# Performance work log

Hardware: AMD Instinct MI355X
Metric: run time of the kernel (lower is better)

The kernel has to match this reference:

```python
import jax, jax.numpy as jnp
import numpy as np

B, NQ, NK, DQ, DK, DV, H = 8, 256, 512, 256, 256, 256, 64
NEG = -1e6


def setup_inputs() -> dict:
    key = jax.random.key(0)
    k1, k2, k3, k4, k5, k6, k7 = jax.random.split(key, 7)
    return {
        "queries": jax.random.normal(k1, (B, NQ, DQ), dtype=jnp.float32),
        "keys": jax.random.normal(k2, (B, NK, DK), dtype=jnp.float32),
        "values": jax.random.normal(k3, (B, NK, DV), dtype=jnp.float32),
        "valid_lens": jax.random.randint(k4, (B,), 1, NK + 1),
        "Wq": jax.random.normal(k5, (DQ, H), dtype=jnp.float32) / np.sqrt(DQ),
        "Wk": jax.random.normal(k6, (DK, H), dtype=jnp.float32) / np.sqrt(DK),
        "wv": jax.random.normal(k7, (H,), dtype=jnp.float32) / np.sqrt(H),
    }


def reference(queries, keys, values, valid_lens, Wq, Wk, wv):
    # project: [B,NQ,H], [B,NK,H]
    q = jnp.einsum("bqd,dh->bqh", queries, Wq)
    k = jnp.einsum("bkd,dh->bkh", keys, Wk)
    # additive features: [B,NQ,NK,H] -> tanh -> reduce with w_v -> scores [B,NQ,NK]
    features = jnp.tanh(q[:, :, None, :] + k[:, None, :, :])
    scores = jnp.einsum("bqkh,h->bqk", features, wv)
    # masked softmax over key axis (per-batch valid_lens)
    mask = jnp.arange(NK)[None, None, :] < valid_lens[:, None, None]
    scores = jnp.where(mask, scores, NEG)
    attn = jax.nn.softmax(scores, axis=-1)
    # dropout p=0 (eval) -> identity; weighted sum of values [B,NQ,DV]
    return jnp.einsum("bqk,bkv->bqv", attn, values)
```

## Files before the change

### kernel.cpp

```cpp
#include <hip/hip_runtime.h>
#include <hip/hip_bf16.h>

constexpr int B  = 8;
constexpr int NQ = 256;
constexpr int NK = 512;
constexpr int D  = 256;
constexpr int DV = 256;
constexpr int H  = 64;
constexpr float NEG = -1e6f;
constexpr float LOG2E = 1.4426950408889634f;
constexpr float CSCALE = 2.f * LOG2E;

constexpr int RPB = 32;

__global__ __launch_bounds__(512) void proj_kernel(
    const float* __restrict__ queries, const float* __restrict__ keys,
    const float* __restrict__ Wq, const float* __restrict__ Wk,
    float* __restrict__ qp, float* __restrict__ kp)
{
    const int r0 = blockIdx.x * RPB;
    const bool isQ = (r0 < B * NQ);
    const float* src = isQ ? queries + (size_t)r0 * D
                           : keys + (size_t)(r0 - B * NQ) * D;
    const float* W   = isQ ? Wq : Wk;
    float* out       = isQ ? qp + (size_t)r0 * H
                           : kp + (size_t)(r0 - B * NQ) * H;

    __shared__ __align__(16) float rows[RPB][D];
#pragma unroll
    for (int j = 0; j < 4; ++j)
        ((float4*)&rows[0][0])[threadIdx.x + j * 512] =
            ((const float4*)src)[threadIdx.x + j * 512];
    __syncthreads();

    const int h = threadIdx.x & 63;
    const int g = threadIdx.x >> 6;
    float s0 = 0.f, s1 = 0.f, s2 = 0.f, s3 = 0.f;
#pragma unroll 2
    for (int d4 = 0; d4 < D / 4; ++d4) {
        float w0 = W[(d4 * 4 + 0) * H + h];
        float w1 = W[(d4 * 4 + 1) * H + h];
        float w2 = W[(d4 * 4 + 2) * H + h];
        float w3 = W[(d4 * 4 + 3) * H + h];
        float4 ra = *(const float4*)&rows[g][d4 * 4];
        float4 rb = *(const float4*)&rows[g + 8][d4 * 4];
        float4 rc = *(const float4*)&rows[g + 16][d4 * 4];
        float4 rd = *(const float4*)&rows[g + 24][d4 * 4];
        s0 = fmaf(ra.x, w0, s0);  s1 = fmaf(rb.x, w0, s1);
        s2 = fmaf(rc.x, w0, s2);  s3 = fmaf(rd.x, w0, s3);
        s0 = fmaf(ra.y, w1, s0);  s1 = fmaf(rb.y, w1, s1);
        s2 = fmaf(rc.y, w1, s2);  s3 = fmaf(rd.y, w1, s3);
        s0 = fmaf(ra.z, w2, s0);  s1 = fmaf(rb.z, w2, s1);
        s2 = fmaf(rc.z, w2, s2);  s3 = fmaf(rd.z, w2, s3);
        s0 = fmaf(ra.w, w3, s0);  s1 = fmaf(rb.w, w3, s1);
        s2 = fmaf(rc.w, w3, s2);  s3 = fmaf(rd.w, w3, s3);
    }
    out[g * H + h]         = s0 * CSCALE;
    out[(g + 8) * H + h]   = s1 * CSCALE;
    out[(g + 16) * H + h]  = s2 * CSCALE;
    out[(g + 24) * H + h]  = s3 * CSCALE;
}

constexpr int KT   = 128;
constexpr int KPAD = 68;

#define FMA4(acc, a, v) \
    acc.x = fmaf(a, v.x, acc.x); acc.y = fmaf(a, v.y, acc.y); \
    acc.z = fmaf(a, v.z, acc.z); acc.w = fmaf(a, v.w, acc.w);

__global__ __launch_bounds__(512, 4) void attn_kernel(
    const float* __restrict__ qp, const float* __restrict__ kp,
    const float* __restrict__ values, const int* __restrict__ valid_lens,
    const float* __restrict__ wv, float* __restrict__ out)
{
    const int b    = blockIdx.x & 7;
    const int q0   = (blockIdx.x >> 3) * 4;
    const int t    = threadIdx.x;
    const int w    = t >> 6;
    const int l    = t & 63;
    const int qloc = w >> 1;
    const int half = w & 1;

    __shared__ __align__(16) float kT[KT * KPAD];
    __shared__ __align__(16) float qv[4][H];
    __shared__ __align__(16) float w2[H];
    __shared__ __align__(16) float sc[4][NK];

    if (half == 0)
        qv[qloc][l] = qp[((size_t)b * NQ + q0 + qloc) * H + l];

    const float wvl = wv[l];
    float swv = wvl;
#pragma unroll
    for (int off = 32; off > 0; off >>= 1) swv += __shfl_xor(swv, off);
    if (w == 0) w2[l] = -2.f * wvl;

    const int vlen = valid_lens[b];

    for (int kt = 0; kt < NK / KT; ++kt) {
        const int kg = kt * KT + half * 64 + l;
        if (kt * KT < vlen) {
            __syncthreads();
            const float* src = kp + ((size_t)b * NK + kt * KT) * H;
#pragma unroll
            for (int j = 0; j < 4; ++j) {
                int idx4 = t + j * 512;
                int kk = idx4 >> 4;
                int hb = (idx4 & 15) * 4;
                float4 v = ((const float4*)src)[idx4];
                *(float4*)&kT[kk * KPAD + hb] = v;
            }
            __syncthreads();

            if (kt * KT + half * 64 < vlen) {
                const float* qrow = &qv[qloc][0];
                const float* krow = &kT[(half * 64 + l) * KPAD];
                float s0 = 0.f;
#pragma unroll
                for (int h4 = 0; h4 < H / 4; ++h4) {
                    float4 qq = *(const float4*)&qrow[h4 * 4];
                    float4 ww = *(const float4*)&w2[h4 * 4];
                    float4 kk = *(const float4*)&krow[h4 * 4];
                    float Ax = __builtin_amdgcn_exp2f(qq.x + kk.x) + 1.f;
                    float Ay = __builtin_amdgcn_exp2f(qq.y + kk.y) + 1.f;
                    float Az = __builtin_amdgcn_exp2f(qq.z + kk.z) + 1.f;
                    float Aw = __builtin_amdgcn_exp2f(qq.w + kk.w) + 1.f;
                    float n1 = fmaf(ww.x, Ay, ww.y * Ax);
                    float d1 = Ax * Ay;
                    float n2 = fmaf(ww.z, Aw, ww.w * Az);
                    float d2 = Az * Aw;
                    float nq = fmaf(n1, d2, n2 * d1);
                    float dq = d1 * d2;
                    s0 = fmaf(nq, __builtin_amdgcn_rcpf(dq), s0);
                }
                sc[qloc][kg] = (kg < vlen) ? (s0 + swv) : NEG;
            } else {
                sc[qloc][kg] = NEG;
            }
        } else {
            sc[qloc][kg] = NEG;
        }
    }
    __syncthreads();

    float vals[8];
    float m = -INFINITY;
#pragma unroll
    for (int j = 0; j < 8; ++j) {
        vals[j] = sc[qloc][l + j * 64];
        m = fmaxf(m, vals[j]);
    }
#pragma unroll
    for (int off = 32; off > 0; off >>= 1) m = fmaxf(m, __shfl_xor(m, off));
    float sum = 0.f;
#pragma unroll
    for (int j = 0; j < 8; ++j) {
        float p = __builtin_amdgcn_exp2f((vals[j] - m) * LOG2E);
        vals[j] = p;
        sum += p;
    }
#pragma unroll
    for (int off = 32; off > 0; off >>= 1) sum += __shfl_xor(sum, off);
    const float rinv = __builtin_amdgcn_rcpf(sum);
    if (half == 0) {
        sc[qloc][l + 0 * 64] = vals[0] * rinv;
        sc[qloc][l + 1 * 64] = vals[1] * rinv;
        sc[qloc][l + 2 * 64] = vals[2] * rinv;
        sc[qloc][l + 3 * 64] = vals[3] * rinv;
    } else {
        sc[qloc][l + 4 * 64] = vals[4] * rinv;
        sc[qloc][l + 5 * 64] = vals[5] * rinv;
        sc[qloc][l + 6 * 64] = vals[6] * rinv;
        sc[qloc][l + 7 * 64] = vals[7] * rinv;
    }
    __syncthreads();

    float4 acc0 = {0,0,0,0}, acc1 = {0,0,0,0}, acc2 = {0,0,0,0}, acc3 = {0,0,0,0};
    const float* Vb = values + (size_t)b * NK * DV;
    const int nchunks = (vlen + 3) >> 2;
    for (int c = w; c < nchunks; c += 8) {
        const int k = 4 * c;
        float4 a0 = *(const float4*)&sc[0][k];
        float4 a1 = *(const float4*)&sc[1][k];
        float4 a2 = *(const float4*)&sc[2][k];
        float4 a3 = *(const float4*)&sc[3][k];
        const float* vr = Vb + (size_t)k * DV + 4 * l;
        float4 v0 = *(const float4*)(vr);
        float4 v1 = *(const float4*)(vr + DV);
        float4 v2 = *(const float4*)(vr + 2 * DV);
        float4 v3 = *(const float4*)(vr + 3 * DV);
        FMA4(acc0, a0.x, v0); FMA4(acc0, a0.y, v1); FMA4(acc0, a0.z, v2); FMA4(acc0, a0.w, v3);
        FMA4(acc1, a1.x, v0); FMA4(acc1, a1.y, v1); FMA4(acc1, a1.z, v2); FMA4(acc1, a1.w, v3);
        FMA4(acc2, a2.x, v0); FMA4(acc2, a2.y, v1); FMA4(acc2, a2.z, v2); FMA4(acc2, a2.w, v3);
        FMA4(acc3, a3.x, v0); FMA4(acc3, a3.y, v1); FMA4(acc3, a3.z, v2); FMA4(acc3, a3.w, v3);
    }

    float* pt = kT;
    *(float4*)&pt[(w * 4 + 0) * 256 + 4 * l] = acc0;
    *(float4*)&pt[(w * 4 + 1) * 256 + 4 * l] = acc1;
    *(float4*)&pt[(w * 4 + 2) * 256 + 4 * l] = acc2;
    *(float4*)&pt[(w * 4 + 3) * 256 + 4 * l] = acc3;
    __syncthreads();

    if (w < 4) {
        float4 r = {0,0,0,0};
#pragma unroll
        for (int s = 0; s < 8; ++s) {
            float4 p = *(const float4*)&pt[(s * 4 + w) * 256 + 4 * l];
            r.x += p.x; r.y += p.y; r.z += p.z; r.w += p.w;
        }
        *(float4*)&out[((size_t)b * NQ + q0 + w) * DV + 4 * l] = r;
    }
}

extern "C" void kernel_launch(void* const* d_in, const int* in_sizes, int n_in,
                              void* d_out, int out_size, void* d_ws, size_t ws_size,
                              hipStream_t stream) {
    const float* queries    = (const float*)d_in[0];
    const float* keys       = (const float*)d_in[1];
    const float* values     = (const float*)d_in[2];
    const int*   valid_lens = (const int*)d_in[3];
    const float* Wq         = (const float*)d_in[4];
    const float* Wk         = (const float*)d_in[5];
    const float* wv         = (const float*)d_in[6];
    float* out = (float*)d_out;

    float* qp = (float*)d_ws;
    float* kp = qp + (size_t)B * NQ * H;

    proj_kernel<<<(B * NQ + B * NK) / RPB, 512, 0, stream>>>(
        queries, keys, Wq, Wk, qp, kp);

    attn_kernel<<<B * (NQ / 4), 512, 0, stream>>>(
        qp, kp, values, valid_lens, wv, out);
}
```

Before: 103.7 us.

## Process eight queries per block with max-free softmax and prefetched key tiles

The attention kernel now runs 1024 threads and handles 8 queries per block, so each key tile and value row loaded is reused across twice as many queries. The softmax drops the max subtraction, relying on the score being bounded by the sum of |wv|. Exponentials are computed in the score loop and normalisation is deferred to the output. Key tiles are register-prefetched for the next iteration and fully masked tiles are skipped. In exchange the kernel uses more registers and barriers, launches fewer blocks, and the unshifted exponent could lose precision if the score bound were large.

```diff
diff --git a/kernel.cpp b/kernel.cpp
--- a/kernel.cpp
+++ b/kernel.cpp
@@ -7,7 +7,6 @@
 constexpr int D  = 256;
 constexpr int DV = 256;
 constexpr int H  = 64;
-constexpr float NEG = -1e6f;
 constexpr float LOG2E = 1.4426950408889634f;
 constexpr float CSCALE = 2.f * LOG2E;
 
@@ -63,18 +62,20 @@
 
 constexpr int KT   = 128;
 constexpr int KPAD = 68;
-
-#define FMA4(acc, a, v) \
-    acc.x = fmaf(a, v.x, acc.x); acc.y = fmaf(a, v.y, acc.y); \
-    acc.z = fmaf(a, v.z, acc.z); acc.w = fmaf(a, v.w, acc.w);
-
-__global__ __launch_bounds__(512, 4) void attn_kernel(
+constexpr int QPB  = 8;
+
+#define FMA2(acc, a, v) \
+    acc.x = fmaf(a, v.x, acc.x); acc.y = fmaf(a, v.y, acc.y);
+#define AVQ(acc, aq) \
+    FMA2(acc, aq.x, v0) FMA2(acc, aq.y, v1) FMA2(acc, aq.z, v2) FMA2(acc, aq.w, v3)
+
+__global__ __launch_bounds__(1024, 4) void attn_kernel(
     const float* __restrict__ qp, const float* __restrict__ kp,
     const float* __restrict__ values, const int* __restrict__ valid_lens,
     const float* __restrict__ wv, float* __restrict__ out)
 {
     const int b    = blockIdx.x & 7;
-    const int q0   = (blockIdx.x >> 3) * 4;
+    const int q0   = (blockIdx.x >> 3) * QPB;
     const int t    = threadIdx.x;
     const int w    = t >> 6;
     const int l    = t & 63;
@@ -82,9 +83,10 @@
     const int half = w & 1;
 
     __shared__ __align__(16) float kT[KT * KPAD];
-    __shared__ __align__(16) float qv[4][H];
+    __shared__ __align__(16) float qv[QPB][H];
     __shared__ __align__(16) float w2[H];
-    __shared__ __align__(16) float sc[4][NK];
+    __shared__ __align__(16) float rq[QPB];
+    __shared__ __align__(16) float sc[QPB][NK];
 
     if (half == 0)
         qv[qloc][l] = qp[((size_t)b * NQ + q0 + qloc) * H + l];
@@ -96,120 +98,124 @@
     if (w == 0) w2[l] = -2.f * wvl;
 
     const int vlen = valid_lens[b];
-
-    for (int kt = 0; kt < NK / KT; ++kt) {
+    const int ntl  = (vlen + KT - 1) / KT;
+
+    for (int kt = ntl; kt < NK / KT; ++kt)
+        sc[qloc][kt * KT + half * 64 + l] = 0.f;
+
+    const float* kb = kp + (size_t)b * NK * H;
+    float4 r0 = ((const float4*)kb)[t];
+    float4 r1 = ((const float4*)kb)[t + 1024];
+
+    for (int kt = 0; kt < ntl; ++kt) {
+        __syncthreads();
+        {
+            int i4 = t;
+            *(float4*)&kT[(i4 >> 4) * KPAD + (i4 & 15) * 4] = r0;
+            i4 = t + 1024;
+            *(float4*)&kT[(i4 >> 4) * KPAD + (i4 & 15) * 4] = r1;
+        }
+        if (kt + 1 < ntl) {
+            const float* nsrc = kb + (size_t)(kt + 1) * KT * H;
+            r0 = ((const float4*)nsrc)[t];
+            r1 = ((const float4*)nsrc)[t + 1024];
+        }
+        __syncthreads();
+
         const int kg = kt * KT + half * 64 + l;
-        if (kt * KT < vlen) {
-            __syncthreads();
-            const float* src = kp + ((size_t)b * NK + kt * KT) * H;
-#pragma unroll
-            for (int j = 0; j < 4; ++j) {
-                int idx4 = t + j * 512;
-                int kk = idx4 >> 4;
-                int hb = (idx4 & 15) * 4;
-                float4 v = ((const float4*)src)[idx4];
-                *(float4*)&kT[kk * KPAD + hb] = v;
+        if (kt * KT + half * 64 < vlen) {
+            const float* qrow = &qv[qloc][0];
+            const float* krow = &kT[(half * 64 + l) * KPAD];
+            float s0 = 0.f;
+#pragma unroll
+            for (int h4 = 0; h4 < H / 4; ++h4) {
+                float4 qq = *(const float4*)&qrow[h4 * 4];
+                float4 ww = *(const float4*)&w2[h4 * 4];
+                float4 kk = *(const float4*)&krow[h4 * 4];
+                float Ax = __builtin_amdgcn_exp2f(qq.x + kk.x) + 1.f;
+                float Ay = __builtin_amdgcn_exp2f(qq.y + kk.y) + 1.f;
+                float Az = __builtin_amdgcn_exp2f(qq.z + kk.z) + 1.f;
+                float Aw = __builtin_amdgcn_exp2f(qq.w + kk.w) + 1.f;
+                float n1 = fmaf(ww.x, Ay, ww.y * Ax);
+                float d1 = Ax * Ay;
+                float n2 = fmaf(ww.z, Aw, ww.w * Az);
+                float d2 = Az * Aw;
+                float nq = fmaf(n1, d2, n2 * d1);
+                float dq = d1 * d2;
+                s0 = fmaf(nq, __builtin_amdgcn_rcpf(dq), s0);
             }
-            __syncthreads();
-
-            if (kt * KT + half * 64 < vlen) {
-                const float* qrow = &qv[qloc][0];
-                const float* krow = &kT[(half * 64 + l) * KPAD];
-                float s0 = 0.f;
-#pragma unroll
-                for (int h4 = 0; h4 < H / 4; ++h4) {
-                    float4 qq = *(const float4*)&qrow[h4 * 4];
-                    float4 ww = *(const float4*)&w2[h4 * 4];
-                    float4 kk = *(const float4*)&krow[h4 * 4];
-                    float Ax = __builtin_amdgcn_exp2f(qq.x + kk.x) + 1.f;
-                    float Ay = __builtin_amdgcn_exp2f(qq.y + kk.y) + 1.f;
-                    float Az = __builtin_amdgcn_exp2f(qq.z + kk.z) + 1.f;
-                    float Aw = __builtin_amdgcn_exp2f(qq.w + kk.w) + 1.f;
-                    float n1 = fmaf(ww.x, Ay, ww.y * Ax);
-                    float d1 = Ax * Ay;
-                    float n2 = fmaf(ww.z, Aw, ww.w * Az);
-                    float d2 = Az * Aw;
-                    float nq = fmaf(n1, d2, n2 * d1);
-                    float dq = d1 * d2;
-                    s0 = fmaf(nq, __builtin_amdgcn_rcpf(dq), s0);
-                }
-                sc[qloc][kg] = (kg < vlen) ? (s0 + swv) : NEG;
-            } else {
-                sc[qloc][kg] = NEG;
-            }
+            sc[qloc][kg] = (kg < vlen)
+                ? __builtin_amdgcn_exp2f((s0 + swv) * LOG2E) : 0.f;
         } else {
-            sc[qloc][kg] = NEG;
-        }
-    }
-    __syncthreads();
-
-    float vals[8];
-    float m = -INFINITY;
-#pragma unroll
-    for (int j = 0; j < 8; ++j) {
-        vals[j] = sc[qloc][l + j * 64];
-        m = fmaxf(m, vals[j]);
-    }
-#pragma unroll
-    for (int off = 32; off > 0; off >>= 1) m = fmaxf(m, __shfl_xor(m, off));
+            sc[qloc][kg] = 0.f;
+        }
+    }
+    __syncthreads();
+
     float sum = 0.f;
 #pragma unroll
-    for (int j = 0; j < 8; ++j) {
-        float p = __builtin_amdgcn_exp2f((vals[j] - m) * LOG2E);
-        vals[j] = p;
-        sum += p;
-    }
+    for (int j = 0; j < 8; ++j) sum += sc[qloc][l + j * 64];
 #pragma unroll
     for (int off = 32; off > 0; off >>= 1) sum += __shfl_xor(sum, off);
-    const float rinv = __builtin_amdgcn_rcpf(sum);
-    if (half == 0) {
-        sc[qloc][l + 0 * 64] = vals[0] * rinv;
-        sc[qloc][l + 1 * 64] = vals[1] * rinv;
-        sc[qloc][l + 2 * 64] = vals[2] * rinv;
-        sc[qloc][l + 3 * 64] = vals[3] * rinv;
-    } else {
-        sc[qloc][l + 4 * 64] = vals[4] * rinv;
-        sc[qloc][l + 5 * 64] = vals[5] * rinv;
-        sc[qloc][l + 6 * 64] = vals[6] * rinv;
-        sc[qloc][l + 7 * 64] = vals[7] * rinv;
-    }
-    __syncthreads();
-
-    float4 acc0 = {0,0,0,0}, acc1 = {0,0,0,0}, acc2 = {0,0,0,0}, acc3 = {0,0,0,0};
-    const float* Vb = values + (size_t)b * NK * DV;
+    if (half == 0 && l == 0) rq[qloc] = __builtin_amdgcn_rcpf(sum);
+
+    float2 acc0{0,0}, acc1{0,0}, acc2{0,0}, acc3{0,0};
+    float2 acc4{0,0}, acc5{0,0}, acc6{0,0}, acc7{0,0};
+    const float* Vb = values + (size_t)b * NK * DV + half * 128 + 2 * l;
     const int nchunks = (vlen + 3) >> 2;
-    for (int c = w; c < nchunks; c += 8) {
+    for (int c = qloc; c < nchunks; c += 8) {
         const int k = 4 * c;
         float4 a0 = *(const float4*)&sc[0][k];
         float4 a1 = *(const float4*)&sc[1][k];
         float4 a2 = *(const float4*)&sc[2][k];
         float4 a3 = *(const float4*)&sc[3][k];
-        const float* vr = Vb + (size_t)k * DV + 4 * l;
-        float4 v0 = *(const float4*)(vr);
-        float4 v1 = *(const float4*)(vr + DV);
-        float4 v2 = *(const float4*)(vr + 2 * DV);
-        float4 v3 = *(const float4*)(vr + 3 * DV);
-        FMA4(acc0, a0.x, v0); FMA4(acc0, a0.y, v1); FMA4(acc0, a0.z, v2); FMA4(acc0, a0.w, v3);
-        FMA4(acc1, a1.x, v0); FMA4(acc1, a1.y, v1); FMA4(acc1, a1.z, v2); FMA4(acc1, a1.w, v3);
-        FMA4(acc2, a2.x, v0); FMA4(acc2, a2.y, v1); FMA4(acc2, a2.z, v2); FMA4(acc2, a2.w, v3);
-        FMA4(acc3, a3.x, v0); FMA4(acc3, a3.y, v1); FMA4(acc3, a3.z, v2); FMA4(acc3, a3.w, v3);
+        float4 a4 = *(const float4*)&sc[4][k];
+        float4 a5 = *(const float4*)&sc[5][k];
+        float4 a6 = *(const float4*)&sc[6][k];
+        float4 a7 = *(const float4*)&sc[7][k];
+        const float* vr = Vb + (size_t)k * DV;
+        float2 v0 = *(const float2*)(vr);
+        float2 v1 = *(const float2*)(vr + DV);
+        float2 v2 = *(const float2*)(vr + 2 * DV);
+        float2 v3 = *(const float2*)(vr + 3 * DV);
+        AVQ(acc0, a0) AVQ(acc1, a1) AVQ(acc2, a2) AVQ(acc3, a3)
+        AVQ(acc4, a4) AVQ(acc5, a5) AVQ(acc6, a6) AVQ(acc7, a7)
     }
 
     float* pt = kT;
-    *(float4*)&pt[(w * 4 + 0) * 256 + 4 * l] = acc0;
-    *(float4*)&pt[(w * 4 + 1) * 256 + 4 * l] = acc1;
-    *(float4*)&pt[(w * 4 + 2) * 256 + 4 * l] = acc2;
-    *(float4*)&pt[(w * 4 + 3) * 256 + 4 * l] = acc3;
-    __syncthreads();
-
+    const int pbase = qloc * 4 * 256 + half * 128 + 2 * l;
+    *(float2*)&pt[pbase + 0 * 256] = acc0;
+    *(float2*)&pt[pbase + 1 * 256] = acc1;
+    *(float2*)&pt[pbase + 2 * 256] = acc2;
+    *(float2*)&pt[pbase + 3 * 256] = acc3;
+    __syncthreads();
     if (w < 4) {
-        float4 r = {0,0,0,0};
-#pragma unroll
-        for (int s = 0; s < 8; ++s) {
-            float4 p = *(const float4*)&pt[(s * 4 + w) * 256 + 4 * l];
-            r.x += p.x; r.y += p.y; r.z += p.z; r.w += p.w;
-        }
+        float4 r{0,0,0,0};
+#pragma unroll
+        for (int p = 0; p < 8; ++p) {
+            float4 x = *(const float4*)&pt[(p * 4 + w) * 256 + 4 * l];
+            r.x += x.x; r.y += x.y; r.z += x.z; r.w += x.w;
+        }
+        const float s = rq[w];
+        r.x *= s; r.y *= s; r.z *= s; r.w *= s;
         *(float4*)&out[((size_t)b * NQ + q0 + w) * DV + 4 * l] = r;
+    }
+    __syncthreads();
+    *(float2*)&pt[pbase + 0 * 256] = acc4;
+    *(float2*)&pt[pbase + 1 * 256] = acc5;
+    *(float2*)&pt[pbase + 2 * 256] = acc6;
+    *(float2*)&pt[pbase + 3 * 256] = acc7;
+    __syncthreads();
+    if (w < 4) {
+        float4 r{0,0,0,0};
+#pragma unroll
+        for (int p = 0; p < 8; ++p) {
+            float4 x = *(const float4*)&pt[(p * 4 + w) * 256 + 4 * l];
+            r.x += x.x; r.y += x.y; r.z += x.z; r.w += x.w;
+        }
+        const float s = rq[4 + w];
+        r.x *= s; r.y *= s; r.z *= s; r.w *= s;
+        *(float4*)&out[((size_t)b * NQ + q0 + 4 + w) * DV + 4 * l] = r;
     }
 }
 
@@ -231,6 +237,6 @@
     proj_kernel<<<(B * NQ + B * NK) / RPB, 512, 0, stream>>>(
         queries, keys, Wq, Wk, qp, kp);
 
-    attn_kernel<<<B * (NQ / 4), 512, 0, stream>>>(
+    attn_kernel<<<B * (NQ / QPB), 1024, 0, stream>>>(
         qp, kp, values, valid_lens, wv, out);
 }
```

Measured after the change: 103.2 us. Within noise of the previous version (-0.4%).
